# Kernel tuning notes

Hardware: AMD Instinct MI355X
Metric: run time of the kernel (lower is better)

Reference implementation:

```python
import jax, jax.numpy as jnp
import numpy as np

FILTER_SIZE = 1024
NUM_HEADS = 16
D_HEAD = FILTER_SIZE // NUM_HEADS
LN_EPS = 1e-5


def setup_inputs() -> dict:
    key = jax.random.key(0)
    ks = jax.random.split(key, 10)
    B, T, D = 2, 2048, FILTER_SIZE
    s = 1.0 / np.sqrt(D)
    return {
        "x": jax.random.normal(ks[0], (B, T, D), dtype=jnp.float32),
        "Wq": jax.random.normal(ks[1], (D, D), dtype=jnp.float32) * s,
        "bq": jnp.zeros((D,), dtype=jnp.float32),
        "Wk": jax.random.normal(ks[2], (D, D), dtype=jnp.float32) * s,
        "bk": jnp.zeros((D,), dtype=jnp.float32),
        "Wv": jax.random.normal(ks[3], (D, D), dtype=jnp.float32) * s,
        "bv": jnp.zeros((D,), dtype=jnp.float32),
        "Wo": jax.random.normal(ks[4], (D, D), dtype=jnp.float32) * s,
        "bo": jnp.zeros((D,), dtype=jnp.float32),
        "gamma": jnp.ones((D,), dtype=jnp.float32),
        "beta": jnp.zeros((D,), dtype=jnp.float32),
    }


def reference(x, Wq, bq, Wk, bk, Wv, bv, Wo, bo, gamma, beta):
    B, T, D = x.shape
    H, Dh = NUM_HEADS, D_HEAD
    # Note: source splits features as (d_head, heads) with heads LAST.
    q = (x @ Wq.T + bq).reshape(B, T, Dh, H)
    k = (x @ Wk.T + bk).reshape(B, T, Dh, H)
    v = (x @ Wv.T + bv).reshape(B, T, Dh, H)
    scale = 1.0 / np.sqrt(Dh).astype(np.float32)
    # scores: (B, H, T, T)
    scores = jnp.einsum("bidh,bjdh->bhij", q, k) * scale
    attn = jax.nn.softmax(scores, axis=-1)  # dropout is identity in eval
    out = jnp.einsum("bhij,bjdh->bidh", attn, v)  # (B, T, Dh, H)
    out = out.reshape(B, T, D)  # matches permute(0,2,3,1).reshape in torch
    out = out @ Wo.T + bo
    out = out + x
    mu = jnp.mean(out, axis=-1, keepdims=True)
    var = jnp.var(out, axis=-1, keepdims=True)
    out = (out - mu) * jax.lax.rsqrt(var + LN_EPS) * gamma + beta
    return out
```

## Files before the change

kernel.cpp:

```cpp
#include <hip/hip_runtime.h>
#include <stdint.h>

#define T_SEQ 2048
#define D_MODEL 1024
#define NH 16
#define DH 64
#define NROWS 4096

typedef __bf16 bf16x8 __attribute__((ext_vector_type(8)));
typedef float floatx4 __attribute__((ext_vector_type(4)));
typedef short short4v __attribute__((ext_vector_type(4)));
typedef short short8v __attribute__((ext_vector_type(8)));

#define AS1 __attribute__((address_space(1)))
#define AS3 __attribute__((address_space(3)))

static __device__ __forceinline__ void gl2lds16(const unsigned short* g, unsigned short* s) {
    __builtin_amdgcn_global_load_lds((const AS1 unsigned int*)g, (AS3 unsigned int*)s, 16, 0, 0);
}

static __device__ __forceinline__ unsigned short f32_bf16(float f) {
    union { float f; unsigned int u; } c; c.f = f;
    unsigned int u = c.u;
    u = u + 0x7FFFu + ((u >> 16) & 1u);
    return (unsigned short)(u >> 16);
}

static __device__ __forceinline__ unsigned int pack2_bf16(float a, float b) {
    return (unsigned int)f32_bf16(a) | ((unsigned int)f32_bf16(b) << 16);
}

static __device__ __forceinline__ floatx4 mfma16(bf16x8 a, bf16x8 b, floatx4 c) {
    return __builtin_amdgcn_mfma_f32_16x16x32_bf16(a, b, c, 0, 0, 0);
}

static __device__ __forceinline__ bf16x8 as_bf(short8v s) {
    union { short8v s; bf16x8 b; } u; u.s = s; return u.b;
}

#define QSCALE 0.1803368801111204f
#define EXP2_SHIFT 10.0f
#define WAITCNT_VM(n) (0x0F70 | (n))

__global__ __launch_bounds__(256) void k_conv_all(const float* __restrict__ x,
                                                  const float* __restrict__ Wq,
                                                  const float* __restrict__ Wk,
                                                  const float* __restrict__ Wv,
                                                  const float* __restrict__ Wo,
                                                  unsigned short* __restrict__ x_bf,
                                                  unsigned short* __restrict__ wqkv_bf,
                                                  unsigned short* __restrict__ wo_bf) {
    int b = blockIdx.x, t = threadIdx.x;
    if (b < 4096) {
        int i = b * 1024 + t * 4;
        float4 v = *(const float4*)(x + i);
        uint2 o;
        o.x = pack2_bf16(v.x, v.y);
        o.y = pack2_bf16(v.z, v.w);
        *(uint2*)(x_bf + i) = o;
    } else if (b < 7168) {
        int idx = b - 4096;
        int tensor = idx >> 10, np = idx & 1023;
        const float* src = tensor == 0 ? Wq : tensor == 1 ? Wk : Wv;
        int f = (np & 63) * 16 + (np >> 6);
        int c = t * 4;
        float4 v = *(const float4*)(src + (long)f * D_MODEL + c);
        uint2 o;
        o.x = pack2_bf16(v.x, v.y);
        o.y = pack2_bf16(v.z, v.w);
        *(uint2*)(wqkv_bf + ((long)tensor * D_MODEL + np) * D_MODEL + c) = o;
    } else {
        int n = b - 7168;
        int fp = t * 4;
        const float* row = Wo + (long)n * D_MODEL;
        unsigned short o[4];
        #pragma unroll
        for (int k = 0; k < 4; k++) {
            int f = fp + k;
            o[k] = f32_bf16(row[(f & 63) * 16 + (f >> 6)]);
        }
        *(uint2*)(wo_bf + (long)n * D_MODEL + fp) = *(const uint2*)o;
    }
}

__global__ __launch_bounds__(512, 2) void k_qkv256(const unsigned short* __restrict__ A,
                                                   const unsigned short* __restrict__ W,
                                                   const float* __restrict__ bq,
                                                   const float* __restrict__ bk,
                                                   const float* __restrict__ bv,
                                                   unsigned short* __restrict__ out_bf,
                                                   unsigned short* __restrict__ vtg) {
    __shared__ unsigned short lds[2 * 32768];
    const int tid = threadIdx.x;
    const int w = tid >> 6, l = tid & 63;
    const int lrow = l & 15, lq = l >> 4;
    const int sw8 = lrow & 7;
    const int wm_id = w >> 2, wn_id = w & 3;
    const int L = blockIdx.x;
    const int bx = (L & 7) * 2 + ((L >> 3) & 1);
    const int by = L >> 4;
    const long am0 = (long)bx * 256;
    const long wn0 = (long)by * 256;

    const int rl = l >> 3;
    const int gl = ((l & 7) ^ rl) * 8;

    floatx4 acc[8][4] = {};

    auto stage_piece = [&](int ki, int sel, int piece) {
        int c = piece & 3;
        int chunk = c * 8 + w;
        int k0 = ki * 64;
        if (piece < 4) {
            gl2lds16(A + (am0 + chunk * 8 + rl) * D_MODEL + k0 + gl,
                     lds + sel * 32768 + chunk * 512);
        } else {
            gl2lds16(W + (wn0 + chunk * 8 + rl) * D_MODEL + k0 + gl,
                     lds + sel * 32768 + 16384 + chunk * 512);
        }
    };

    #pragma unroll
    for (int pc = 0; pc < 8; pc++) stage_piece(0, 0, pc);
    __builtin_amdgcn_s_waitcnt(WAITCNT_VM(0));
    __builtin_amdgcn_s_barrier();

    for (int t = 0; t < 16; t++) {
        const int sel = t & 1;
        const unsigned short* Ab = lds + sel * 32768;
        const unsigned short* Bb = Ab + 16384;
        bf16x8 bfr[4];
        #pragma unroll
        for (int q = 0; q < 4; q++) {
            const int ks = q >> 1, mh = q & 1;
            if (mh == 0) {
                #pragma unroll
                for (int nt = 0; nt < 4; nt++) {
                    int row = wn_id * 64 + nt * 16 + lrow;
                    bfr[nt] = *(const bf16x8*)(Bb + row * 64 + (((ks * 4 + lq) ^ sw8) * 8));
                }
            }
            bf16x8 af[4];
            #pragma unroll
            for (int j = 0; j < 4; j++) {
                int row = wm_id * 128 + (mh * 4 + j) * 16 + lrow;
                af[j] = *(const bf16x8*)(Ab + row * 64 + (((ks * 4 + lq) ^ sw8) * 8));
            }
            if (t < 15) {
                if (q == 0) {
                    stage_piece(t + 1, sel ^ 1, 0);
                    stage_piece(t + 1, sel ^ 1, 1);
                    stage_piece(t + 1, sel ^ 1, 2);
                } else if (q == 1) {
                    stage_piece(t + 1, sel ^ 1, 3);
                    stage_piece(t + 1, sel ^ 1, 4);
                    stage_piece(t + 1, sel ^ 1, 5);
                } else if (q == 2) {
                    stage_piece(t + 1, sel ^ 1, 6);
                    stage_piece(t + 1, sel ^ 1, 7);
                }
            }
            __builtin_amdgcn_s_barrier();
            __builtin_amdgcn_s_setprio(1);
            #pragma unroll
            for (int j = 0; j < 4; j++)
                #pragma unroll
                for (int nt = 0; nt < 4; nt++)
                    acc[mh * 4 + j][nt] = mfma16(af[j], bfr[nt], acc[mh * 4 + j][nt]);
            __builtin_amdgcn_s_setprio(0);
            if (q == 3 && t < 15)
                __builtin_amdgcn_s_waitcnt(WAITCNT_VM(0));
            __builtin_amdgcn_s_barrier();
        }
    }

    int tensor = by >> 2;
    int nbase = (by & 3) * 256;
    const float* bias = tensor == 0 ? bq : tensor == 1 ? bk : bv;
    float scale = tensor == 0 ? QSCALE : 1.0f;
    if (tensor < 2) {
        unsigned short* outt = out_bf + (size_t)tensor * (32u * T_SEQ * DH);
        #pragma unroll
        for (int mt = 0; mt < 8; mt++) {
            #pragma unroll
            for (int nt = 0; nt < 4; nt++) {
                int n = nbase + wn_id * 64 + nt * 16 + lrow;
                int h = n >> 6, d = n & 63;
                float bb = bias[d * 16 + h];
                #pragma unroll
                for (int r = 0; r < 4; r++) {
                    int row = (int)am0 + wm_id * 128 + mt * 16 + lq * 4 + r;
                    float v = (acc[mt][nt][r] + bb) * scale;
                    int b = row >> 11, i = row & 2047;
                    long idx = ((long)(b * 16 + h) * T_SEQ + i) * DH + d;
                    outt[idx] = f32_bf16(v);
                }
            }
        }
    } else {
        int row0 = (int)am0 + wm_id * 128;
        int b = row0 >> 11;
        int blkb = (row0 & 2047) >> 6;
        #pragma unroll
        for (int nt = 0; nt < 4; nt++) {
            int n = nbase + wn_id * 64 + nt * 16 + lrow;
            int h = n >> 6, d = n & 63;
            float bb = bias[d * 16 + h];
            #pragma unroll
            for (int mt = 0; mt < 8; mt++) {
                int blk = blkb + (mt >> 2);
                int m4 = mt & 3;
                long base = (((long)(b * 16 + h) * 64 + d) * 32 + blk) * 64;
                uint2 o;
                o.x = pack2_bf16(acc[mt][nt][0] + bb, acc[mt][nt][1] + bb);
                o.y = pack2_bf16(acc[mt][nt][2] + bb, acc[mt][nt][3] + bb);
                *(uint2*)(vtg + base + (m4 >> 1) * 32 + lq * 8 + (m4 & 1) * 4) = o;
            }
        }
    }
}

template <int BN, int MODE>
__global__ __launch_bounds__(256) void k_gemm(const unsigned short* __restrict__ A,
                                              const unsigned short* __restrict__ W,
                                              const float* __restrict__ b0,
                                              const float* __restrict__ resid,
                                              float* __restrict__ out_f32) {
    constexpr int NT = BN / 32;
    constexpr int NCB = BN / 32;
    constexpr int NDMA = 4 + NCB;
    __shared__ unsigned short lds_a[2 * 128 * 64];
    __shared__ unsigned short lds_b[2 * BN * 64];
    const int tid = threadIdx.x;
    const int w = tid >> 6, l = tid & 63;
    const int lrow = l & 15, lq = l >> 4;
    const int wm = (w >> 1) * 64, wn = (w & 1) * (BN / 2);
    const int L = blockIdx.x;
    const int bx = (L & 7) * 4 + ((L >> 3) & 3);
    const int by = L >> 5;
    const long am0 = (long)bx * 128;
    const long wn0 = (long)by * BN;

    floatx4 acc[4][NT] = {};
    const int grow = l >> 3;
    const int gcol = ((l & 7) ^ grow) * 8;
    const int sw8 = (lrow & 7);

    auto stage = [&](int ki, int sel) {
        unsigned short* la = lds_a + sel * 8192;
        unsigned short* lb = lds_b + sel * (BN * 64);
        int k0 = ki * 64;
        #pragma unroll
        for (int c = 0; c < 4; c++) {
            int chunk = w * 4 + c;
            gl2lds16(A + (am0 + chunk * 8 + grow) * D_MODEL + k0 + gcol, la + chunk * 512);
        }
        #pragma unroll
        for (int c = 0; c < NCB; c++) {
            int chunk = w * NCB + c;
            gl2lds16(W + (wn0 + chunk * 8 + grow) * D_MODEL + k0 + gcol, lb + chunk * 512);
        }
    };

    auto compute = [&](const unsigned short* la, const unsigned short* lb) {
        bf16x8 af[4][2], bfr[NT][2];
        #pragma unroll
        for (int mt = 0; mt < 4; mt++)
            #pragma unroll
            for (int ks = 0; ks < 2; ks++)
                af[mt][ks] = *(const bf16x8*)(la + (wm + mt * 16 + lrow) * 64 +
                                              (((ks * 4 + lq) ^ sw8) * 8));
        #pragma unroll
        for (int nt = 0; nt < NT; nt++)
            #pragma unroll
            for (int ks = 0; ks < 2; ks++)
                bfr[nt][ks] = *(const bf16x8*)(lb + (wn + nt * 16 + lrow) * 64 +
                                               (((ks * 4 + lq) ^ sw8) * 8));
        #pragma unroll
        for (int mt = 0; mt < 4; mt++)
            #pragma unroll
            for (int nt = 0; nt < NT; nt++)
                #pragma unroll
                for (int ks = 0; ks < 2; ks++)
                    acc[mt][nt] = mfma16(af[mt][ks], bfr[nt][ks], acc[mt][nt]);
    };

    stage(0, 0);
    for (int i = 0; i < 16; i++) {
        const int cur = i & 1;
        if (i < 15) {
            stage(i + 1, 1 - cur);
            __builtin_amdgcn_s_waitcnt(WAITCNT_VM(NDMA));
        } else {
            __builtin_amdgcn_s_waitcnt(WAITCNT_VM(0));
        }
        __builtin_amdgcn_s_barrier();
        compute(lds_a + cur * 8192, lds_b + cur * (BN * 64));
        __builtin_amdgcn_s_barrier();
    }

    #pragma unroll
    for (int mt = 0; mt < 4; mt++) {
        #pragma unroll
        for (int nt = 0; nt < NT; nt++) {
            int n = (int)wn0 + wn + nt * 16 + lrow;
            float bb = b0[n];
            #pragma unroll
            for (int r = 0; r < 4; r++) {
                int row = (int)am0 + wm + mt * 16 + lq * 4 + r;
                long idx = (long)row * D_MODEL + n;
                out_f32[idx] = acc[mt][nt][r] + bb + resid[idx];
            }
        }
    }
}

__global__ __launch_bounds__(256) void k_attn(const unsigned short* __restrict__ q_ws,
                                              const unsigned short* __restrict__ k_ws,
                                              const unsigned short* __restrict__ vtg,
                                              unsigned short* __restrict__ att) {
    __shared__ unsigned short kbuf[2 * 64 * 64];
    __shared__ unsigned short vbuf[2 * 64 * 64];
    const int tid = threadIdx.x;
    const int w = tid >> 6, l = tid & 63;
    const int lrow = l & 15, lq = l >> 4;
    const int sw = lrow & 7;
    const int L = blockIdx.x;
    const int bh = (L & 7) * 4 + ((L >> 3) & 3);
    const int i0 = (L >> 5) * 128;
    const unsigned short* kh = k_ws + (long)bh * T_SEQ * DH;
    const unsigned short* vh = vtg + (long)bh * 64 * T_SEQ;

    const int rl = l >> 3;
    const int gl = ((l & 7) ^ rl) * 8;

    bf16x8 qf[2][2];
    #pragma unroll
    for (int qt = 0; qt < 2; qt++) {
        const unsigned short* qp =
            q_ws + ((long)bh * T_SEQ + i0 + w * 32 + qt * 16 + lrow) * DH + lq * 8;
        qf[qt][0] = *(const bf16x8*)qp;
        qf[qt][1] = *(const bf16x8*)(qp + 32);
    }
    floatx4 o_acc[2][4] = {};
    floatx4 l_acc[2] = {};
    const short8v ones8s = {0x3F80, 0x3F80, 0x3F80, 0x3F80, 0x3F80, 0x3F80, 0x3F80, 0x3F80};
    const bf16x8 ones8 = as_bf(ones8s);

    auto stage_k = [&](int jt, int sel) {
        unsigned short* kd = kbuf + sel * 4096 + (w * 2) * 512;
        #pragma unroll
        for (int c = 0; c < 2; c++) {
            int row = w * 16 + c * 8 + rl;
            gl2lds16(kh + ((long)(jt * 64 + row)) * 64 + gl, kd + c * 512);
        }
    };
    auto stage_v = [&](int jt, int sel) {
        unsigned short* vd = vbuf + sel * 4096 + (w * 2) * 512;
        #pragma unroll
        for (int c = 0; c < 2; c++) {
            int row = w * 16 + c * 8 + rl;
            gl2lds16(vh + ((long)row * 32 + jt) * 64 + gl, vd + c * 512);
        }
    };

    auto qk = [&](const unsigned short* kb_, floatx4 (&s0)[4], floatx4 (&s1)[4]) {
        #pragma unroll
        for (int nt = 0; nt < 4; nt++) {
            const unsigned short* kp = kb_ + (nt * 16 + lrow) * 64;
            bf16x8 ka = *(const bf16x8*)(kp + ((lq ^ sw) * 8));
            bf16x8 kb = *(const bf16x8*)(kp + (((lq + 4) ^ sw) * 8));
            floatx4 c0 = {-EXP2_SHIFT, -EXP2_SHIFT, -EXP2_SHIFT, -EXP2_SHIFT};
            floatx4 c1 = c0;
            c0 = mfma16(ka, qf[0][0], c0);
            c0 = mfma16(kb, qf[0][1], c0);
            c1 = mfma16(ka, qf[1][0], c1);
            c1 = mfma16(kb, qf[1][1], c1);
            s0[nt] = c0;
            s1[nt] = c1;
        }
    };

    auto sp4 = [&](floatx4 s) -> short4v {
        float p0 = __builtin_amdgcn_exp2f(s[0]);
        float p1 = __builtin_amdgcn_exp2f(s[1]);
        float p2 = __builtin_amdgcn_exp2f(s[2]);
        float p3 = __builtin_amdgcn_exp2f(s[3]);
        uint2 pk;
        pk.x = __builtin_amdgcn_perm(__float_as_uint(p1), __float_as_uint(p0), 0x07060302);
        pk.y = __builtin_amdgcn_perm(__float_as_uint(p3), __float_as_uint(p2), 0x07060302);
        union { uint2 u; short4v s4; } cv; cv.u = pk;
        return cv.s4;
    };

    auto pv_dt = [&](const unsigned short* vb_, int dt,
                     short8v (&p0)[2], short8v (&p1)[2]) {
        const unsigned short* vp = vb_ + (dt * 16 + lrow) * 64;
        bf16x8 vg0 = *(const bf16x8*)(vp + ((lq ^ sw) * 8));
        bf16x8 vg1 = *(const bf16x8*)(vp + (((4 + lq) ^ sw) * 8));
        o_acc[0][dt] = mfma16(vg0, as_bf(p0[0]), o_acc[0][dt]);
        o_acc[0][dt] = mfma16(vg1, as_bf(p0[1]), o_acc[0][dt]);
        o_acc[1][dt] = mfma16(vg0, as_bf(p1[0]), o_acc[1][dt]);
        o_acc[1][dt] = mfma16(vg1, as_bf(p1[1]), o_acc[1][dt]);
    };

    auto tile_body = [&](const unsigned short* kb_, const unsigned short* vb_,
                         short8v (&pp0)[2], short8v (&pp1)[2],
                         short8v (&pc0)[2], short8v (&pc1)[2]) {
        floatx4 s0[4], s1[4];
        qk(kb_, s0, s1);
        #pragma unroll
        for (int g = 0; g < 2; g++) {
            pv_dt(vb_, 2 * g, pp0, pp1);
            short4v t00 = sp4(s0[2 * g]);
            short4v t10 = sp4(s1[2 * g]);
            pv_dt(vb_, 2 * g + 1, pp0, pp1);
            short4v t01 = sp4(s0[2 * g + 1]);
            short4v t11 = sp4(s1[2 * g + 1]);
            pc0[g] = __builtin_shufflevector(t00, t01, 0, 1, 2, 3, 4, 5, 6, 7);
            pc1[g] = __builtin_shufflevector(t10, t11, 0, 1, 2, 3, 4, 5, 6, 7);
            l_acc[0] = mfma16(ones8, as_bf(pc0[g]), l_acc[0]);
            l_acc[1] = mfma16(ones8, as_bf(pc1[g]), l_acc[1]);
        }
    };

    short8v pA0[2], pA1[2], pB0[2], pB1[2];

    stage_k(0, 0);
    stage_k(1, 1);
    stage_v(0, 0);
    __builtin_amdgcn_s_waitcnt(WAITCNT_VM(4));
    __builtin_amdgcn_s_barrier();
    {
        floatx4 s0[4], s1[4];
        qk(kbuf, s0, s1);
        #pragma unroll
        for (int g = 0; g < 2; g++) {
            short4v t00 = sp4(s0[2 * g]);
            short4v t01 = sp4(s0[2 * g + 1]);
            short4v t10 = sp4(s1[2 * g]);
            short4v t11 = sp4(s1[2 * g + 1]);
            pA0[g] = __builtin_shufflevector(t00, t01, 0, 1, 2, 3, 4, 5, 6, 7);
            pA1[g] = __builtin_shufflevector(t10, t11, 0, 1, 2, 3, 4, 5, 6, 7);
            l_acc[0] = mfma16(ones8, as_bf(pA0[g]), l_acc[0]);
            l_acc[1] = mfma16(ones8, as_bf(pA1[g]), l_acc[1]);
        }
    }
    __builtin_amdgcn_s_barrier();

    for (int t = 1; t < 31; t += 2) {
        stage_k(t + 1, (t + 1) & 1);
        stage_v(t, t & 1);
        __builtin_amdgcn_s_waitcnt(WAITCNT_VM(4));
        __builtin_amdgcn_s_barrier();
        tile_body(kbuf + (t & 1) * 4096, vbuf + ((t - 1) & 1) * 4096,
                  pA0, pA1, pB0, pB1);
        __builtin_amdgcn_s_barrier();
        stage_k(t + 2, t & 1);
        stage_v(t + 1, (t + 1) & 1);
        __builtin_amdgcn_s_waitcnt(WAITCNT_VM(4));
        __builtin_amdgcn_s_barrier();
        tile_body(kbuf + ((t + 1) & 1) * 4096, vbuf + (t & 1) * 4096,
                  pB0, pB1, pA0, pA1);
        __builtin_amdgcn_s_barrier();
    }

    stage_v(31, 1);
    __builtin_amdgcn_s_waitcnt(WAITCNT_VM(2));
    __builtin_amdgcn_s_barrier();
    tile_body(kbuf + 4096, vbuf + 0, pA0, pA1, pB0, pB1);
    __builtin_amdgcn_s_barrier();

    __builtin_amdgcn_s_waitcnt(WAITCNT_VM(0));
    __builtin_amdgcn_s_barrier();
    #pragma unroll
    for (int dt = 0; dt < 4; dt++) pv_dt(vbuf + 4096, dt, pB0, pB1);

    int h = bh & 15, b = bh >> 4;
    #pragma unroll
    for (int qt = 0; qt < 2; qt++) {
        float rl2 = 1.0f / l_acc[qt][0];
        int i = i0 + w * 32 + qt * 16 + lrow;
        unsigned short* orow = att + ((long)(b * T_SEQ + i)) * D_MODEL + h * 64;
        #pragma unroll
        for (int dt = 0; dt < 4; dt++) {
            uint2 o;
            o.x = pack2_bf16(o_acc[qt][dt][0] * rl2, o_acc[qt][dt][1] * rl2);
            o.y = pack2_bf16(o_acc[qt][dt][2] * rl2, o_acc[qt][dt][3] * rl2);
            *(uint2*)(orow + dt * 16 + lq * 4) = o;
        }
    }
}

__global__ __launch_bounds__(256) void k_ln(float* __restrict__ io,
                                            const float* __restrict__ gamma,
                                            const float* __restrict__ beta) {
    int row = blockIdx.x, t = threadIdx.x;
    float* p = io + (long)row * D_MODEL + t * 4;
    float4 v = *(float4*)p;
    float s = v.x + v.y + v.z + v.w;
    float ss = v.x * v.x + v.y * v.y + v.z * v.z + v.w * v.w;
    #pragma unroll
    for (int m = 1; m < 64; m <<= 1) {
        s += __shfl_xor(s, m);
        ss += __shfl_xor(ss, m);
    }
    __shared__ float red[8];
    if ((t & 63) == 0) { red[t >> 6] = s; red[4 + (t >> 6)] = ss; }
    __syncthreads();
    s = red[0] + red[1] + red[2] + red[3];
    ss = red[4] + red[5] + red[6] + red[7];
    float mu = s * (1.0f / 1024.0f);
    float var = ss * (1.0f / 1024.0f) - mu * mu;
    float rstd = rsqrtf(var + 1e-5f);
    float4 g = *(const float4*)(gamma + t * 4);
    float4 be = *(const float4*)(beta + t * 4);
    float4 o;
    o.x = (v.x - mu) * rstd * g.x + be.x;
    o.y = (v.y - mu) * rstd * g.y + be.y;
    o.z = (v.z - mu) * rstd * g.z + be.z;
    o.w = (v.w - mu) * rstd * g.w + be.w;
    *(float4*)p = o;
}

extern "C" void kernel_launch(void* const* d_in, const int* in_sizes, int n_in,
                              void* d_out, int out_size, void* d_ws, size_t ws_size,
                              hipStream_t stream) {
    const float* x = (const float*)d_in[0];
    const float* Wq = (const float*)d_in[1];
    const float* bq = (const float*)d_in[2];
    const float* Wk = (const float*)d_in[3];
    const float* bk = (const float*)d_in[4];
    const float* Wv = (const float*)d_in[5];
    const float* bv = (const float*)d_in[6];
    const float* Wo = (const float*)d_in[7];
    const float* bo = (const float*)d_in[8];
    const float* gamma = (const float*)d_in[9];
    const float* beta = (const float*)d_in[10];
    float* out = (float*)d_out;

    char* ws = (char*)d_ws;
    unsigned short* x_bf = (unsigned short*)(ws);
    unsigned short* wqkv_bf = (unsigned short*)(ws + ((size_t)8 << 20));
    unsigned short* wo_bf = (unsigned short*)(ws + ((size_t)14 << 20));
    unsigned short* qkv_ws = (unsigned short*)(ws + ((size_t)16 << 20));
    unsigned short* att = x_bf;

    unsigned short* q_ws = qkv_ws;
    unsigned short* k_ws = qkv_ws + (size_t)32 * T_SEQ * DH;
    unsigned short* vtg = qkv_ws + (size_t)64 * T_SEQ * DH;

    k_conv_all<<<8192, 256, 0, stream>>>(x, Wq, Wk, Wv, Wo, x_bf, wqkv_bf, wo_bf);

    k_qkv256<<<192, 512, 0, stream>>>(x_bf, wqkv_bf, bq, bk, bv, qkv_ws, vtg);

    k_attn<<<512, 256, 0, stream>>>(q_ws, k_ws, vtg, att);

    k_gemm<64, 1><<<512, 256, 0, stream>>>(
        att, wo_bf, bo, x, out);

    k_ln<<<NROWS, 256, 0, stream>>>(out, gamma, beta);
}
```

Baseline: 195.7 us.

## Restructure attention K/V staging to 4-deep ring and drop software-pipelined PV

The attention kernel now stages K and V together into a 4-slot LDS ring, prefetching two tiles ahead with a single barrier per tile. It replaces the previous software pipeline, which overlapped one tile's PV with the next tile's QK/exp, with a straightforward per-tile QK, exp and PV sequence. LDS usage doubles and cross-tile overlap of MFMA and exp is lost. The QKV GEMM also issues all eight stage pieces at the first sub-step instead of spreading them across three.

```diff
diff --git a/kernel.cpp b/kernel.cpp
--- a/kernel.cpp
+++ b/kernel.cpp
@@ -146,19 +146,9 @@
                 int row = wm_id * 128 + (mh * 4 + j) * 16 + lrow;
                 af[j] = *(const bf16x8*)(Ab + row * 64 + (((ks * 4 + lq) ^ sw8) * 8));
             }
-            if (t < 15) {
-                if (q == 0) {
-                    stage_piece(t + 1, sel ^ 1, 0);
-                    stage_piece(t + 1, sel ^ 1, 1);
-                    stage_piece(t + 1, sel ^ 1, 2);
-                } else if (q == 1) {
-                    stage_piece(t + 1, sel ^ 1, 3);
-                    stage_piece(t + 1, sel ^ 1, 4);
-                    stage_piece(t + 1, sel ^ 1, 5);
-                } else if (q == 2) {
-                    stage_piece(t + 1, sel ^ 1, 6);
-                    stage_piece(t + 1, sel ^ 1, 7);
-                }
+            if (t < 15 && q == 0) {
+                #pragma unroll
+                for (int pc = 0; pc < 8; pc++) stage_piece(t + 1, sel ^ 1, pc);
             }
             __builtin_amdgcn_s_barrier();
             __builtin_amdgcn_s_setprio(1);
@@ -319,8 +309,8 @@
                                               const unsigned short* __restrict__ k_ws,
                                               const unsigned short* __restrict__ vtg,
                                               unsigned short* __restrict__ att) {
-    __shared__ unsigned short kbuf[2 * 64 * 64];
-    __shared__ unsigned short vbuf[2 * 64 * 64];
+    __shared__ unsigned short kbuf[4 * 4096];
+    __shared__ unsigned short vbuf[4 * 4096];
     const int tid = threadIdx.x;
     const int w = tid >> 6, l = tid & 63;
     const int lrow = l & 15, lq = l >> 4;
@@ -347,37 +337,18 @@
     const short8v ones8s = {0x3F80, 0x3F80, 0x3F80, 0x3F80, 0x3F80, 0x3F80, 0x3F80, 0x3F80};
     const bf16x8 ones8 = as_bf(ones8s);
 
-    auto stage_k = [&](int jt, int sel) {
+    auto stage = [&](int jt, int sel) {
         unsigned short* kd = kbuf + sel * 4096 + (w * 2) * 512;
+        unsigned short* vd = vbuf + sel * 4096 + (w * 2) * 512;
         #pragma unroll
         for (int c = 0; c < 2; c++) {
             int row = w * 16 + c * 8 + rl;
             gl2lds16(kh + ((long)(jt * 64 + row)) * 64 + gl, kd + c * 512);
         }
-    };
-    auto stage_v = [&](int jt, int sel) {
-        unsigned short* vd = vbuf + sel * 4096 + (w * 2) * 512;
         #pragma unroll
         for (int c = 0; c < 2; c++) {
             int row = w * 16 + c * 8 + rl;
             gl2lds16(vh + ((long)row * 32 + jt) * 64 + gl, vd + c * 512);
-        }
-    };
-
-    auto qk = [&](const unsigned short* kb_, floatx4 (&s0)[4], floatx4 (&s1)[4]) {
-        #pragma unroll
-        for (int nt = 0; nt < 4; nt++) {
-            const unsigned short* kp = kb_ + (nt * 16 + lrow) * 64;
-            bf16x8 ka = *(const bf16x8*)(kp + ((lq ^ sw) * 8));
-            bf16x8 kb = *(const bf16x8*)(kp + (((lq + 4) ^ sw) * 8));
-            floatx4 c0 = {-EXP2_SHIFT, -EXP2_SHIFT, -EXP2_SHIFT, -EXP2_SHIFT};
-            floatx4 c1 = c0;
-            c0 = mfma16(ka, qf[0][0], c0);
-            c0 = mfma16(kb, qf[0][1], c0);
-            c1 = mfma16(ka, qf[1][0], c1);
-            c1 = mfma16(kb, qf[1][1], c1);
-            s0[nt] = c0;
-            s1[nt] = c1;
         }
     };
 
@@ -404,77 +375,57 @@
         o_acc[1][dt] = mfma16(vg1, as_bf(p1[1]), o_acc[1][dt]);
     };
 
-    auto tile_body = [&](const unsigned short* kb_, const unsigned short* vb_,
-                         short8v (&pp0)[2], short8v (&pp1)[2],
-                         short8v (&pc0)[2], short8v (&pc1)[2]) {
+    stage(0, 0);
+    stage(1, 1);
+
+    for (int t = 0; t < 32; t++) {
+        const int sl = t & 3;
+        if (t < 30) stage(t + 2, (t + 2) & 3);
+        if (t < 30)
+            __builtin_amdgcn_s_waitcnt(WAITCNT_VM(8));
+        else if (t == 30)
+            __builtin_amdgcn_s_waitcnt(WAITCNT_VM(4));
+        else
+            __builtin_amdgcn_s_waitcnt(WAITCNT_VM(0));
+        __builtin_amdgcn_s_barrier();
+
+        const unsigned short* kb_ = kbuf + sl * 4096;
+        const unsigned short* vb_ = vbuf + sl * 4096;
+
         floatx4 s0[4], s1[4];
-        qk(kb_, s0, s1);
-        #pragma unroll
-        for (int g = 0; g < 2; g++) {
-            pv_dt(vb_, 2 * g, pp0, pp1);
-            short4v t00 = sp4(s0[2 * g]);
-            short4v t10 = sp4(s1[2 * g]);
-            pv_dt(vb_, 2 * g + 1, pp0, pp1);
-            short4v t01 = sp4(s0[2 * g + 1]);
-            short4v t11 = sp4(s1[2 * g + 1]);
-            pc0[g] = __builtin_shufflevector(t00, t01, 0, 1, 2, 3, 4, 5, 6, 7);
-            pc1[g] = __builtin_shufflevector(t10, t11, 0, 1, 2, 3, 4, 5, 6, 7);
-            l_acc[0] = mfma16(ones8, as_bf(pc0[g]), l_acc[0]);
-            l_acc[1] = mfma16(ones8, as_bf(pc1[g]), l_acc[1]);
-        }
-    };
-
-    short8v pA0[2], pA1[2], pB0[2], pB1[2];
-
-    stage_k(0, 0);
-    stage_k(1, 1);
-    stage_v(0, 0);
-    __builtin_amdgcn_s_waitcnt(WAITCNT_VM(4));
-    __builtin_amdgcn_s_barrier();
-    {
-        floatx4 s0[4], s1[4];
-        qk(kbuf, s0, s1);
-        #pragma unroll
-        for (int g = 0; g < 2; g++) {
-            short4v t00 = sp4(s0[2 * g]);
-            short4v t01 = sp4(s0[2 * g + 1]);
-            short4v t10 = sp4(s1[2 * g]);
-            short4v t11 = sp4(s1[2 * g + 1]);
-            pA0[g] = __builtin_shufflevector(t00, t01, 0, 1, 2, 3, 4, 5, 6, 7);
-            pA1[g] = __builtin_shufflevector(t10, t11, 0, 1, 2, 3, 4, 5, 6, 7);
-            l_acc[0] = mfma16(ones8, as_bf(pA0[g]), l_acc[0]);
-            l_acc[1] = mfma16(ones8, as_bf(pA1[g]), l_acc[1]);
-        }
-    }
-    __builtin_amdgcn_s_barrier();
-
-    for (int t = 1; t < 31; t += 2) {
-        stage_k(t + 1, (t + 1) & 1);
-        stage_v(t, t & 1);
-        __builtin_amdgcn_s_waitcnt(WAITCNT_VM(4));
-        __builtin_amdgcn_s_barrier();
-        tile_body(kbuf + (t & 1) * 4096, vbuf + ((t - 1) & 1) * 4096,
-                  pA0, pA1, pB0, pB1);
-        __builtin_amdgcn_s_barrier();
-        stage_k(t + 2, t & 1);
-        stage_v(t + 1, (t + 1) & 1);
-        __builtin_amdgcn_s_waitcnt(WAITCNT_VM(4));
-        __builtin_amdgcn_s_barrier();
-        tile_body(kbuf + ((t + 1) & 1) * 4096, vbuf + (t & 1) * 4096,
-                  pB0, pB1, pA0, pA1);
-        __builtin_amdgcn_s_barrier();
-    }
-
-    stage_v(31, 1);
-    __builtin_amdgcn_s_waitcnt(WAITCNT_VM(2));
-    __builtin_amdgcn_s_barrier();
-    tile_body(kbuf + 4096, vbuf + 0, pA0, pA1, pB0, pB1);
-    __builtin_amdgcn_s_barrier();
-
-    __builtin_amdgcn_s_waitcnt(WAITCNT_VM(0));
-    __builtin_amdgcn_s_barrier();
-    #pragma unroll
-    for (int dt = 0; dt < 4; dt++) pv_dt(vbuf + 4096, dt, pB0, pB1);
+        short4v u0[4], u1[4];
+        #pragma unroll
+        for (int nt = 0; nt < 4; nt++) {
+            const unsigned short* kp = kb_ + (nt * 16 + lrow) * 64;
+            bf16x8 ka = *(const bf16x8*)(kp + ((lq ^ sw) * 8));
+            bf16x8 kb2 = *(const bf16x8*)(kp + (((lq + 4) ^ sw) * 8));
+            floatx4 c0 = {-EXP2_SHIFT, -EXP2_SHIFT, -EXP2_SHIFT, -EXP2_SHIFT};
+            floatx4 c1 = c0;
+            c0 = mfma16(ka, qf[0][0], c0);
+            c0 = mfma16(kb2, qf[0][1], c0);
+            c1 = mfma16(ka, qf[1][0], c1);
+            c1 = mfma16(kb2, qf[1][1], c1);
+            s0[nt] = c0;
+            s1[nt] = c1;
+            if (nt > 0) {
+                u0[nt - 1] = sp4(s0[nt - 1]);
+                u1[nt - 1] = sp4(s1[nt - 1]);
+            }
+        }
+        u0[3] = sp4(s0[3]);
+        u1[3] = sp4(s1[3]);
+        short8v pf0[2], pf1[2];
+        pf0[0] = __builtin_shufflevector(u0[0], u0[1], 0, 1, 2, 3, 4, 5, 6, 7);
+        pf0[1] = __builtin_shufflevector(u0[2], u0[3], 0, 1, 2, 3, 4, 5, 6, 7);
+        pf1[0] = __builtin_shufflevector(u1[0], u1[1], 0, 1, 2, 3, 4, 5, 6, 7);
+        pf1[1] = __builtin_shufflevector(u1[2], u1[3], 0, 1, 2, 3, 4, 5, 6, 7);
+        l_acc[0] = mfma16(ones8, as_bf(pf0[0]), l_acc[0]);
+        l_acc[0] = mfma16(ones8, as_bf(pf0[1]), l_acc[0]);
+        l_acc[1] = mfma16(ones8, as_bf(pf1[0]), l_acc[1]);
+        l_acc[1] = mfma16(ones8, as_bf(pf1[1]), l_acc[1]);
+        #pragma unroll
+        for (int dt = 0; dt < 4; dt++) pv_dt(vb_, dt, pf0, pf1);
+    }
 
     int h = bh & 15, b = bh >> 4;
     #pragma unroll
```

New measurement: 197.9 us. Within noise of the previous version (+1.1%).

## Use four-stage LDS ring for K/V in attention to drop per-tile barriers

Applied to the files above, without the earlier changes.

The attention kernel's K and V LDS buffers grow from double to quadruple buffering. K and V for the same tile are now staged together, prefetched two tiles ahead, and the trailing barrier after each tile body is removed, leaving one barrier per tile. The tile body is also reordered so all PV MFMAs and exp conversions are interleaved first, with the row-sum MFMAs grouped at the end. This doubles LDS use per block (64 KB total), which may lower occupancy, and relies on the deeper ring to keep buffer reuse safe without the extra barriers.

```diff
diff --git a/kernel.cpp b/kernel.cpp
--- a/kernel.cpp
+++ b/kernel.cpp
@@ -319,8 +319,8 @@
                                               const unsigned short* __restrict__ k_ws,
                                               const unsigned short* __restrict__ vtg,
                                               unsigned short* __restrict__ att) {
-    __shared__ unsigned short kbuf[2 * 64 * 64];
-    __shared__ unsigned short vbuf[2 * 64 * 64];
+    __shared__ unsigned short kbuf[4 * 4096];
+    __shared__ unsigned short vbuf[4 * 4096];
     const int tid = threadIdx.x;
     const int w = tid >> 6, l = tid & 63;
     const int lrow = l & 15, lq = l >> 4;
@@ -347,37 +347,18 @@
     const short8v ones8s = {0x3F80, 0x3F80, 0x3F80, 0x3F80, 0x3F80, 0x3F80, 0x3F80, 0x3F80};
     const bf16x8 ones8 = as_bf(ones8s);
 
-    auto stage_k = [&](int jt, int sel) {
+    auto stage = [&](int jt, int sel) {
         unsigned short* kd = kbuf + sel * 4096 + (w * 2) * 512;
+        unsigned short* vd = vbuf + sel * 4096 + (w * 2) * 512;
         #pragma unroll
         for (int c = 0; c < 2; c++) {
             int row = w * 16 + c * 8 + rl;
             gl2lds16(kh + ((long)(jt * 64 + row)) * 64 + gl, kd + c * 512);
         }
-    };
-    auto stage_v = [&](int jt, int sel) {
-        unsigned short* vd = vbuf + sel * 4096 + (w * 2) * 512;
         #pragma unroll
         for (int c = 0; c < 2; c++) {
             int row = w * 16 + c * 8 + rl;
             gl2lds16(vh + ((long)row * 32 + jt) * 64 + gl, vd + c * 512);
-        }
-    };
-
-    auto qk = [&](const unsigned short* kb_, floatx4 (&s0)[4], floatx4 (&s1)[4]) {
-        #pragma unroll
-        for (int nt = 0; nt < 4; nt++) {
-            const unsigned short* kp = kb_ + (nt * 16 + lrow) * 64;
-            bf16x8 ka = *(const bf16x8*)(kp + ((lq ^ sw) * 8));
-            bf16x8 kb = *(const bf16x8*)(kp + (((lq + 4) ^ sw) * 8));
-            floatx4 c0 = {-EXP2_SHIFT, -EXP2_SHIFT, -EXP2_SHIFT, -EXP2_SHIFT};
-            floatx4 c1 = c0;
-            c0 = mfma16(ka, qf[0][0], c0);
-            c0 = mfma16(kb, qf[0][1], c0);
-            c1 = mfma16(ka, qf[1][0], c1);
-            c1 = mfma16(kb, qf[1][1], c1);
-            s0[nt] = c0;
-            s1[nt] = c1;
         }
     };
 
@@ -404,77 +385,90 @@
         o_acc[1][dt] = mfma16(vg1, as_bf(p1[1]), o_acc[1][dt]);
     };
 
-    auto tile_body = [&](const unsigned short* kb_, const unsigned short* vb_,
-                         short8v (&pp0)[2], short8v (&pp1)[2],
-                         short8v (&pc0)[2], short8v (&pc1)[2]) {
+    auto qk = [&](const unsigned short* kb_, floatx4 (&s0)[4], floatx4 (&s1)[4]) {
+        #pragma unroll
+        for (int nt = 0; nt < 4; nt++) {
+            const unsigned short* kp = kb_ + (nt * 16 + lrow) * 64;
+            bf16x8 ka = *(const bf16x8*)(kp + ((lq ^ sw) * 8));
+            bf16x8 kb2 = *(const bf16x8*)(kp + (((lq + 4) ^ sw) * 8));
+            floatx4 c0 = {-EXP2_SHIFT, -EXP2_SHIFT, -EXP2_SHIFT, -EXP2_SHIFT};
+            floatx4 c1 = c0;
+            c0 = mfma16(ka, qf[0][0], c0);
+            c0 = mfma16(kb2, qf[0][1], c0);
+            c1 = mfma16(ka, qf[1][0], c1);
+            c1 = mfma16(kb2, qf[1][1], c1);
+            s0[nt] = c0;
+            s1[nt] = c1;
+        }
+    };
+
+    auto body = [&](const unsigned short* kb_, const unsigned short* vb_,
+                    short8v (&pp0)[2], short8v (&pp1)[2],
+                    short8v (&pc0)[2], short8v (&pc1)[2]) {
         floatx4 s0[4], s1[4];
         qk(kb_, s0, s1);
-        #pragma unroll
-        for (int g = 0; g < 2; g++) {
-            pv_dt(vb_, 2 * g, pp0, pp1);
-            short4v t00 = sp4(s0[2 * g]);
-            short4v t10 = sp4(s1[2 * g]);
-            pv_dt(vb_, 2 * g + 1, pp0, pp1);
-            short4v t01 = sp4(s0[2 * g + 1]);
-            short4v t11 = sp4(s1[2 * g + 1]);
-            pc0[g] = __builtin_shufflevector(t00, t01, 0, 1, 2, 3, 4, 5, 6, 7);
-            pc1[g] = __builtin_shufflevector(t10, t11, 0, 1, 2, 3, 4, 5, 6, 7);
-            l_acc[0] = mfma16(ones8, as_bf(pc0[g]), l_acc[0]);
-            l_acc[1] = mfma16(ones8, as_bf(pc1[g]), l_acc[1]);
-        }
+        short4v u0[4], u1[4];
+        #pragma unroll
+        for (int dt = 0; dt < 4; dt++) {
+            pv_dt(vb_, dt, pp0, pp1);
+            u0[dt] = sp4(s0[dt]);
+            u1[dt] = sp4(s1[dt]);
+        }
+        pc0[0] = __builtin_shufflevector(u0[0], u0[1], 0, 1, 2, 3, 4, 5, 6, 7);
+        pc0[1] = __builtin_shufflevector(u0[2], u0[3], 0, 1, 2, 3, 4, 5, 6, 7);
+        pc1[0] = __builtin_shufflevector(u1[0], u1[1], 0, 1, 2, 3, 4, 5, 6, 7);
+        pc1[1] = __builtin_shufflevector(u1[2], u1[3], 0, 1, 2, 3, 4, 5, 6, 7);
+        l_acc[0] = mfma16(ones8, as_bf(pc0[0]), l_acc[0]);
+        l_acc[0] = mfma16(ones8, as_bf(pc0[1]), l_acc[0]);
+        l_acc[1] = mfma16(ones8, as_bf(pc1[0]), l_acc[1]);
+        l_acc[1] = mfma16(ones8, as_bf(pc1[1]), l_acc[1]);
     };
 
     short8v pA0[2], pA1[2], pB0[2], pB1[2];
 
-    stage_k(0, 0);
-    stage_k(1, 1);
-    stage_v(0, 0);
+    stage(0, 0);
+    stage(1, 1);
     __builtin_amdgcn_s_waitcnt(WAITCNT_VM(4));
     __builtin_amdgcn_s_barrier();
     {
         floatx4 s0[4], s1[4];
         qk(kbuf, s0, s1);
-        #pragma unroll
-        for (int g = 0; g < 2; g++) {
-            short4v t00 = sp4(s0[2 * g]);
-            short4v t01 = sp4(s0[2 * g + 1]);
-            short4v t10 = sp4(s1[2 * g]);
-            short4v t11 = sp4(s1[2 * g + 1]);
-            pA0[g] = __builtin_shufflevector(t00, t01, 0, 1, 2, 3, 4, 5, 6, 7);
-            pA1[g] = __builtin_shufflevector(t10, t11, 0, 1, 2, 3, 4, 5, 6, 7);
-            l_acc[0] = mfma16(ones8, as_bf(pA0[g]), l_acc[0]);
-            l_acc[1] = mfma16(ones8, as_bf(pA1[g]), l_acc[1]);
-        }
-    }
-    __builtin_amdgcn_s_barrier();
+        short4v u0[4], u1[4];
+        #pragma unroll
+        for (int dt = 0; dt < 4; dt++) {
+            u0[dt] = sp4(s0[dt]);
+            u1[dt] = sp4(s1[dt]);
+        }
+        pA0[0] = __builtin_shufflevector(u0[0], u0[1], 0, 1, 2, 3, 4, 5, 6, 7);
+        pA0[1] = __builtin_shufflevector(u0[2], u0[3], 0, 1, 2, 3, 4, 5, 6, 7);
+        pA1[0] = __builtin_shufflevector(u1[0], u1[1], 0, 1, 2, 3, 4, 5, 6, 7);
+        pA1[1] = __builtin_shufflevector(u1[2], u1[3], 0, 1, 2, 3, 4, 5, 6, 7);
+        l_acc[0] = mfma16(ones8, as_bf(pA0[0]), l_acc[0]);
+        l_acc[0] = mfma16(ones8, as_bf(pA0[1]), l_acc[0]);
+        l_acc[1] = mfma16(ones8, as_bf(pA1[0]), l_acc[1]);
+        l_acc[1] = mfma16(ones8, as_bf(pA1[1]), l_acc[1]);
+    }
+    stage(2, 2);
 
     for (int t = 1; t < 31; t += 2) {
-        stage_k(t + 1, (t + 1) & 1);
-        stage_v(t, t & 1);
         __builtin_amdgcn_s_waitcnt(WAITCNT_VM(4));
         __builtin_amdgcn_s_barrier();
-        tile_body(kbuf + (t & 1) * 4096, vbuf + ((t - 1) & 1) * 4096,
-                  pA0, pA1, pB0, pB1);
-        __builtin_amdgcn_s_barrier();
-        stage_k(t + 2, t & 1);
-        stage_v(t + 1, (t + 1) & 1);
+        body(kbuf + (t & 3) * 4096, vbuf + ((t - 1) & 3) * 4096,
+             pA0, pA1, pB0, pB1);
+        stage(t + 2, (t + 2) & 3);
         __builtin_amdgcn_s_waitcnt(WAITCNT_VM(4));
         __builtin_amdgcn_s_barrier();
-        tile_body(kbuf + ((t + 1) & 1) * 4096, vbuf + (t & 1) * 4096,
-                  pB0, pB1, pA0, pA1);
-        __builtin_amdgcn_s_barrier();
-    }
-
-    stage_v(31, 1);
-    __builtin_amdgcn_s_waitcnt(WAITCNT_VM(2));
-    __builtin_amdgcn_s_barrier();
-    tile_body(kbuf + 4096, vbuf + 0, pA0, pA1, pB0, pB1);
-    __builtin_amdgcn_s_barrier();
+        body(kbuf + ((t + 1) & 3) * 4096, vbuf + (t & 3) * 4096,
+             pB0, pB1, pA0, pA1);
+        if (t < 29) stage(t + 3, (t + 3) & 3);
+    }
 
     __builtin_amdgcn_s_waitcnt(WAITCNT_VM(0));
     __builtin_amdgcn_s_barrier();
+    body(kbuf + (31 & 3) * 4096, vbuf + (30 & 3) * 4096, pA0, pA1, pB0, pB1);
+
     #pragma unroll
-    for (int dt = 0; dt < 4; dt++) pv_dt(vbuf + 4096, dt, pB0, pB1);
+    for (int dt = 0; dt < 4; dt++) pv_dt(vbuf + (31 & 3) * 4096, dt, pB0, pB1);
 
     int h = bh & 15, b = bh >> 4;
     #pragma unroll
```

After: 199.4 us. Within noise of the previous version (+1.9%).
